# Kernel optimization log

Measured on AMD Instinct MI355X. Metric: run time of the kernel, lower is better.

## Reference

```python
import jax, jax.numpy as jnp
import numpy as np


def setup_inputs() -> dict:
    key = jax.random.key(0)
    ks = jax.random.split(key, 6)
    B, d, S = 256, 512, 196  # batch, hidden dim, spatial locations (14x14)
    return {
        "memory_state": jax.random.normal(ks[0], (B, d), dtype=jnp.float32),
        "ctrl_state": jax.random.normal(ks[1], (B, d), dtype=jnp.float32),
        "kb_proj": jax.random.normal(ks[2], (B, d, S), dtype=jnp.float32),
        "W_concat": jax.random.normal(ks[3], (d, d), dtype=jnp.float32) * (1.0 / np.sqrt(d)),
        "b_concat": jax.random.normal(ks[4], (d,), dtype=jnp.float32) * 0.01,
        "w_attn": jax.random.normal(ks[5], (d,), dtype=jnp.float32) * (1.0 / np.sqrt(d)),
    }


def reference(memory_state, ctrl_state, kb_proj, W_concat, b_concat, w_attn):
    # I_elements: [B, S, d] -- elementwise gating of knowledge base by memory
    I_t = memory_state[:, :, None] * kb_proj           # [B, d, S]
    I_t = jnp.transpose(I_t, (0, 2, 1))                # [B, S, d]
    # concat_layer (torch Linear: x @ W^T + b) + residual with kb_proj
    concat = jnp.einsum('bsd,ed->bse', I_t, W_concat) + b_concat
    concat = concat + jnp.transpose(kb_proj, (0, 2, 1))  # [B, S, d]
    # attention logits: (concat * ctrl) @ w_attn -> [B, S]
    rai = jnp.einsum('bsd,d->bs', concat * ctrl_state[:, None, :], w_attn)
    rvi = jax.nn.softmax(rai, axis=1)                  # [B, S]
    # attention-weighted sum over spatial locations -> [B, d]
    read_vector = jnp.einsum('bs,bds->bd', rvi, kb_proj)
    return read_vector
```

## Files before the change

kernel.cpp:

```cpp
#include <hip/hip_runtime.h>
#include <math.h>

#define B 256
#define D 512
#define S 196
#define NCH 8
#define TC 16
#define NT 13
#define PAD 20

#define BAR() do { asm volatile("s_waitcnt lgkmcnt(0)" ::: "memory"); \
                   __builtin_amdgcn_s_barrier();                      \
                   asm volatile("" ::: "memory"); } while (0)

__global__ __launch_bounds__(256) void k_gemm2(
    const float* __restrict__ ctrl, const float* __restrict__ w_attn,
    const float* __restrict__ W, float* __restrict__ gpart) {
    __shared__ float u_s[64][8];
    const int ce = blockIdx.x >> 6;
    const int dh = (blockIdx.x >> 5) & 1;
    const int b0 = (blockIdx.x & 31) * 8;
    const int t = threadIdx.x;
    const int d = dh * 256 + t;
#pragma unroll
    for (int k = t; k < 512; k += 256) {
        const int j = k & 7, el = k >> 3;
        const int e = ce * 64 + el;
        u_s[el][j] = ctrl[(size_t)(b0 + j) * D + e] * w_attn[e];
    }
    __syncthreads();
    float a[8];
#pragma unroll
    for (int j = 0; j < 8; ++j) a[j] = 0.f;
    for (int e0 = 0; e0 < 64; e0 += 4) {
        float wv[4];
#pragma unroll
        for (int i = 0; i < 4; ++i)
            wv[i] = W[(size_t)(ce * 64 + e0 + i) * D + d];
#pragma unroll
        for (int i = 0; i < 4; ++i) {
            const float4 ua = *(const float4*)&u_s[e0 + i][0];
            const float4 ub = *(const float4*)&u_s[e0 + i][4];
            a[0] += ua.x * wv[i]; a[1] += ua.y * wv[i];
            a[2] += ua.z * wv[i]; a[3] += ua.w * wv[i];
            a[4] += ub.x * wv[i]; a[5] += ub.y * wv[i];
            a[6] += ub.z * wv[i]; a[7] += ub.w * wv[i];
        }
    }
#pragma unroll
    for (int j = 0; j < 8; ++j)
        gpart[((size_t)(b0 + j) * NCH + ce) * D + d] = a[j];
}

__global__ __launch_bounds__(1024, 1) void k_online(
    const float* __restrict__ kb, const float* __restrict__ gpart,
    const float* __restrict__ mem, const float* __restrict__ ctrl,
    const float* __restrict__ w_attn, float* __restrict__ out) {
    __shared__ __align__(16) float tile[2][D][PAD];
    __shared__ __align__(16) float pr[TC][132];
    __shared__ __align__(16) float w_s[TC];
    __shared__ float p_s[D];
    __shared__ float oa[2][D];
    __shared__ float Zs[2];
    const int b = blockIdx.x;
    const int t = threadIdx.x;
    const float* base = kb + (size_t)b * D * S;

    const int ld_d = t >> 2, col_lo = 4 * (t & 3);

    float4 v0 = *(const float4*)(base + (size_t)ld_d * S + col_lo);
    float4 v1 = *(const float4*)(base + (size_t)(ld_d + 256) * S + col_lo);

    if (t < D) {
        float s = 0.f;
#pragma unroll
        for (int ce = 0; ce < NCH; ++ce)
            s += gpart[((size_t)b * NCH + ce) * D + t];
        p_s[t] = mem[(size_t)b * D + t] * s +
                 ctrl[(size_t)b * D + t] * w_attn[t];
    }
    *(float4*)&tile[0][ld_d][col_lo] = v0;
    *(float4*)&tile[0][ld_d + 256][col_lo] = v1;

    float4 rAa = *(const float4*)(base + (size_t)ld_d * S + TC + col_lo);
    float4 rAb = *(const float4*)(base + (size_t)(ld_d + 256) * S + TC + col_lo);
    float4 rBa = *(const float4*)(base + (size_t)ld_d * S + 2 * TC + col_lo);
    float4 rBb = *(const float4*)(base + (size_t)(ld_d + 256) * S + 2 * TC + col_lo);

    BAR();

    const int c2 = t & 7, dg = t >> 3;
    const float pv0 = p_s[dg * 4 + 0], pv1 = p_s[dg * 4 + 1];
    const float pv2 = p_s[dg * 4 + 2], pv3 = p_s[dg * 4 + 3];
    const int dow = t >> 1, sh = t & 1;

    float Zrun = 0.f, oacc = 0.f;

#define BODY(J, CUR, Ra, Rb)                                                  \
    do {                                                                      \
                                    \
        const float2 q0 = *(const float2*)&tile[CUR][dg * 4 + 0][2 * c2];     \
        const float2 q1 = *(const float2*)&tile[CUR][dg * 4 + 1][2 * c2];     \
        const float2 q2 = *(const float2*)&tile[CUR][dg * 4 + 2][2 * c2];     \
        const float2 q3 = *(const float2*)&tile[CUR][dg * 4 + 3][2 * c2];     \
        pr[2 * c2 + 0][dg] =                                                  \
            pv0 * q0.x + pv1 * q1.x + pv2 * q2.x + pv3 * q3.x;                \
        pr[2 * c2 + 1][dg] =                                                  \
            pv0 * q0.y + pv1 * q1.y + pv2 * q2.y + pv3 * q3.y;                \
        BAR();                                                                \
                          \
        if (t < 64) {                                                         \
            const int c = t >> 2, q = t & 3;                                  \
            float s = 0.f;                                                    \
            _Pragma("unroll")                                                 \
            for (int k = 0; k < 8; ++k) {                                     \
                const float4 v = *(const float4*)&pr[c][q * 32 + 4 * k];      \
                s += (v.x + v.y) + (v.z + v.w);                               \
            }                                                                 \
            s += __shfl_xor(s, 1, 64);                                        \
            s += __shfl_xor(s, 2, 64);                                        \
            if (q == 0) w_s[c] = ((J) * TC + c < S) ? __expf(s) : 0.f;        \
        }                                                                     \
        BAR();                                                                \
                          \
        const float4 wA = *(const float4*)&w_s[sh * 8];                       \
        const float4 wB = *(const float4*)&w_s[sh * 8 + 4];                   \
        Zrun += ((wA.x + wA.y) + (wA.z + wA.w)) +                             \
                ((wB.x + wB.y) + (wB.z + wB.w));                              \
        const float4 ta = *(const float4*)&tile[CUR][dow][sh * 8];            \
        const float4 tb = *(const float4*)&tile[CUR][dow][sh * 8 + 4];        \
        oacc += wA.x * ta.x + wA.y * ta.y + wA.z * ta.z + wA.w * ta.w +       \
                wB.x * tb.x + wB.y * tb.y + wB.z * tb.z + wB.w * tb.w;        \
                      \
        if ((J) + 1 < NT) {                                                   \
            *(float4*)&tile[(CUR) ^ 1][ld_d][col_lo] = Ra;                    \
            *(float4*)&tile[(CUR) ^ 1][ld_d + 256][col_lo] = Rb;              \
        }                                                                     \
        if ((J) + 3 < NT) {                                                   \
            const int cq = ((J) + 3) * TC + col_lo;                           \
            if (cq + 3 < S) {                                                 \
                Ra = *(const float4*)(base + (size_t)ld_d * S + cq);          \
                Rb = *(const float4*)(base + (size_t)(ld_d + 256) * S + cq);  \
            } else {                                                          \
                Ra = make_float4(0.f, 0.f, 0.f, 0.f);                         \
                Rb = make_float4(0.f, 0.f, 0.f, 0.f);                         \
            }                                                                 \
        }                                                                     \
        BAR();                                                                \
    } while (0)

    for (int j = 0; j < NT; j += 2) {
        BODY(j, 0, rAa, rAb);
        if (j + 1 < NT) BODY(j + 1, 1, rBa, rBb);
    }
#undef BODY

    oa[sh][dow] = oacc;
    if (t == 0) Zs[0] = Zrun;
    if (t == 1) Zs[1] = Zrun;
    __syncthreads();
    if (t < D)
        out[(size_t)b * D + t] = (oa[0][t] + oa[1][t]) / (Zs[0] + Zs[1]);
}

extern "C" void kernel_launch(void* const* d_in, const int* in_sizes, int n_in,
                              void* d_out, int out_size, void* d_ws, size_t ws_size,
                              hipStream_t stream) {
    const float* mem  = (const float*)d_in[0];
    const float* ctrl = (const float*)d_in[1];
    const float* kb   = (const float*)d_in[2];
    const float* W    = (const float*)d_in[3];
    const float* wat  = (const float*)d_in[5];
    float* out = (float*)d_out;

    float* gpart = (float*)d_ws;

    k_gemm2 <<<512, 256,  0, stream>>>(ctrl, wat, W, gpart);
    k_online<<<B,   1024, 0, stream>>>(kb, gpart, mem, ctrl, wat, out);
}
```

Before: 175.4 us.

## Split spatial axis across two blocks per batch with merge kernel and register-resident tiles

The online-softmax kernel is split so that each batch is handled by two blocks, each covering half of the spatial locations (7 and 6 chunks), and partial outputs and normalizers go to workspace. A new small kernel merges them by summing the partials and dividing. The weighted-sum stage now reads kb values kept in registers instead of the LDS tile, and the LDS tile is single-buffered with padding, so each block needs far less shared memory. The intent is to get more blocks in flight on the GPU, with one extra launch and partial-result traffic as the added cost.

Measured after the change: 228.1 us. 30.0% more time.

```diff
diff --git a/kernel.cpp b/kernel.cpp
--- a/kernel.cpp
+++ b/kernel.cpp
@@ -6,8 +6,8 @@
 #define S 196
 #define NCH 8
 #define TC 16
-#define NT 13
-#define PAD 20
+#define RPAD 17
+#define PPAD 68
 
 #define BAR() do { asm volatile("s_waitcnt lgkmcnt(0)" ::: "memory"); \
                    __builtin_amdgcn_s_barrier();                      \
@@ -52,24 +52,29 @@
         gpart[((size_t)(b0 + j) * NCH + ce) * D + d] = a[j];
 }
 
-__global__ __launch_bounds__(1024, 1) void k_online(
+__global__ __launch_bounds__(1024, 8) void k_half2(
     const float* __restrict__ kb, const float* __restrict__ gpart,
     const float* __restrict__ mem, const float* __restrict__ ctrl,
-    const float* __restrict__ w_attn, float* __restrict__ out) {
-    __shared__ __align__(16) float tile[2][D][PAD];
-    __shared__ __align__(16) float pr[TC][132];
+    const float* __restrict__ w_attn, float* __restrict__ opart,
+    float* __restrict__ zpart) {
+    __shared__ float tile[D][RPAD];
+    __shared__ float pr[TC][PPAD];
+    __shared__ float p_s[D];
     __shared__ __align__(16) float w_s[TC];
-    __shared__ float p_s[D];
-    __shared__ float oa[2][D];
-    __shared__ float Zs[2];
-    const int b = blockIdx.x;
+    const int bid = blockIdx.x;
+    const int b = bid >> 1, h = bid & 1;
+    const int c0 = h ? 112 : 0;
+    const int NTb = h ? 6 : 7;
     const int t = threadIdx.x;
-    const float* base = kb + (size_t)b * D * S;
+    const float* base = kb + (size_t)b * D * S + c0;
 
     const int ld_d = t >> 2, col_lo = 4 * (t & 3);
+    const int col = t & 15, dseg = t >> 4;
 
-    float4 v0 = *(const float4*)(base + (size_t)ld_d * S + col_lo);
-    float4 v1 = *(const float4*)(base + (size_t)(ld_d + 256) * S + col_lo);
+    float4 vA0 = *(const float4*)(base + (size_t)ld_d * S + col_lo);
+    float4 vA1 = *(const float4*)(base + (size_t)(ld_d + 256) * S + col_lo);
+    float4 vB0 = *(const float4*)(base + (size_t)ld_d * S + TC + col_lo);
+    float4 vB1 = *(const float4*)(base + (size_t)(ld_d + 256) * S + TC + col_lo);
 
     if (t < D) {
         float s = 0.f;
@@ -79,88 +84,97 @@
         p_s[t] = mem[(size_t)b * D + t] * s +
                  ctrl[(size_t)b * D + t] * w_attn[t];
     }
-    *(float4*)&tile[0][ld_d][col_lo] = v0;
-    *(float4*)&tile[0][ld_d + 256][col_lo] = v1;
-
-    float4 rAa = *(const float4*)(base + (size_t)ld_d * S + TC + col_lo);
-    float4 rAb = *(const float4*)(base + (size_t)(ld_d + 256) * S + TC + col_lo);
-    float4 rBa = *(const float4*)(base + (size_t)ld_d * S + 2 * TC + col_lo);
-    float4 rBb = *(const float4*)(base + (size_t)(ld_d + 256) * S + 2 * TC + col_lo);
-
+    tile[ld_d][col_lo + 0] = vA0.x; tile[ld_d][col_lo + 1] = vA0.y;
+    tile[ld_d][col_lo + 2] = vA0.z; tile[ld_d][col_lo + 3] = vA0.w;
+    tile[ld_d + 256][col_lo + 0] = vA1.x; tile[ld_d + 256][col_lo + 1] = vA1.y;
+    tile[ld_d + 256][col_lo + 2] = vA1.z; tile[ld_d + 256][col_lo + 3] = vA1.w;
     BAR();
 
-    const int c2 = t & 7, dg = t >> 3;
-    const float pv0 = p_s[dg * 4 + 0], pv1 = p_s[dg * 4 + 1];
-    const float pv2 = p_s[dg * 4 + 2], pv3 = p_s[dg * 4 + 3];
-    const int dow = t >> 1, sh = t & 1;
+    float pv[8];
+#pragma unroll
+    for (int i = 0; i < 8; ++i) pv[i] = p_s[dseg * 8 + i];
 
-    float Zrun = 0.f, oacc = 0.f;
+    float oacc0 = 0.f, oacc1 = 0.f, Zpart = 0.f;
 
-#define BODY(J, CUR, Ra, Rb)                                                  \
-    do {                                                                      \
-                                    \
-        const float2 q0 = *(const float2*)&tile[CUR][dg * 4 + 0][2 * c2];     \
-        const float2 q1 = *(const float2*)&tile[CUR][dg * 4 + 1][2 * c2];     \
-        const float2 q2 = *(const float2*)&tile[CUR][dg * 4 + 2][2 * c2];     \
-        const float2 q3 = *(const float2*)&tile[CUR][dg * 4 + 3][2 * c2];     \
-        pr[2 * c2 + 0][dg] =                                                  \
-            pv0 * q0.x + pv1 * q1.x + pv2 * q2.x + pv3 * q3.x;                \
-        pr[2 * c2 + 1][dg] =                                                  \
-            pv0 * q0.y + pv1 * q1.y + pv2 * q2.y + pv3 * q3.y;                \
-        BAR();                                                                \
-                          \
-        if (t < 64) {                                                         \
-            const int c = t >> 2, q = t & 3;                                  \
-            float s = 0.f;                                                    \
-            _Pragma("unroll")                                                 \
-            for (int k = 0; k < 8; ++k) {                                     \
-                const float4 v = *(const float4*)&pr[c][q * 32 + 4 * k];      \
-                s += (v.x + v.y) + (v.z + v.w);                               \
-            }                                                                 \
-            s += __shfl_xor(s, 1, 64);                                        \
-            s += __shfl_xor(s, 2, 64);                                        \
-            if (q == 0) w_s[c] = ((J) * TC + c < S) ? __expf(s) : 0.f;        \
-        }                                                                     \
-        BAR();                                                                \
-                          \
-        const float4 wA = *(const float4*)&w_s[sh * 8];                       \
-        const float4 wB = *(const float4*)&w_s[sh * 8 + 4];                   \
-        Zrun += ((wA.x + wA.y) + (wA.z + wA.w)) +                             \
-                ((wB.x + wB.y) + (wB.z + wB.w));                              \
-        const float4 ta = *(const float4*)&tile[CUR][dow][sh * 8];            \
-        const float4 tb = *(const float4*)&tile[CUR][dow][sh * 8 + 4];        \
-        oacc += wA.x * ta.x + wA.y * ta.y + wA.z * ta.z + wA.w * ta.w +       \
-                wB.x * tb.x + wB.y * tb.y + wB.z * tb.z + wB.w * tb.w;        \
-                      \
-        if ((J) + 1 < NT) {                                                   \
-            *(float4*)&tile[(CUR) ^ 1][ld_d][col_lo] = Ra;                    \
-            *(float4*)&tile[(CUR) ^ 1][ld_d + 256][col_lo] = Rb;              \
-        }                                                                     \
-        if ((J) + 3 < NT) {                                                   \
-            const int cq = ((J) + 3) * TC + col_lo;                           \
-            if (cq + 3 < S) {                                                 \
-                Ra = *(const float4*)(base + (size_t)ld_d * S + cq);          \
-                Rb = *(const float4*)(base + (size_t)(ld_d + 256) * S + cq);  \
-            } else {                                                          \
-                Ra = make_float4(0.f, 0.f, 0.f, 0.f);                         \
-                Rb = make_float4(0.f, 0.f, 0.f, 0.f);                         \
-            }                                                                 \
-        }                                                                     \
-        BAR();                                                                \
+#define BODY(J, Oa0, Oa1, Pb0, Pb1)                                          \
+    do {                                                                     \
+            \
+        float a = 0.f;                                                       \
+        _Pragma("unroll")                                                    \
+        for (int i = 0; i < 8; ++i) a += pv[i] * tile[dseg * 8 + i][col];    \
+        pr[col][dseg] = a;                                                   \
+        BAR();                                                               \
+          \
+        if (t < 64) {                                                        \
+            const int c = t >> 2, qq = t & 3;                                \
+            const float4 x0 = *(const float4*)&pr[c][qq * 16 + 0];           \
+            const float4 x1 = *(const float4*)&pr[c][qq * 16 + 4];           \
+            const float4 x2 = *(const float4*)&pr[c][qq * 16 + 8];           \
+            const float4 x3 = *(const float4*)&pr[c][qq * 16 + 12];          \
+            float s = ((x0.x + x0.y) + (x0.z + x0.w)) +                      \
+                      ((x1.x + x1.y) + (x1.z + x1.w)) +                      \
+                      ((x2.x + x2.y) + (x2.z + x2.w)) +                      \
+                      ((x3.x + x3.y) + (x3.z + x3.w));                       \
+            s += __shfl_xor(s, 1, 64);                                       \
+            s += __shfl_xor(s, 2, 64);                                       \
+            if (qq == 0)                                                     \
+                w_s[c] = (c0 + (J) * TC + c < S) ? __expf(s) : 0.f;          \
+        }                                                                    \
+        if ((J) + 1 < NTb) {                                                 \
+            tile[ld_d][col_lo + 0] = Pb0.x; tile[ld_d][col_lo + 1] = Pb0.y;  \
+            tile[ld_d][col_lo + 2] = Pb0.z; tile[ld_d][col_lo + 3] = Pb0.w;  \
+            tile[ld_d + 256][col_lo + 0] = Pb1.x;                            \
+            tile[ld_d + 256][col_lo + 1] = Pb1.y;                            \
+            tile[ld_d + 256][col_lo + 2] = Pb1.z;                            \
+            tile[ld_d + 256][col_lo + 3] = Pb1.w;                            \
+        }                                                                    \
+        BAR();                                                               \
+                    \
+        {                                                                    \
+            const float4 w4 = *(const float4*)&w_s[col_lo];                  \
+            Zpart += (w4.x + w4.y) + (w4.z + w4.w);                          \
+            oacc0 += w4.x * Oa0.x + w4.y * Oa0.y +                           \
+                     w4.z * Oa0.z + w4.w * Oa0.w;                            \
+            oacc1 += w4.x * Oa1.x + w4.y * Oa1.y +                           \
+                     w4.z * Oa1.z + w4.w * Oa1.w;                            \
+        }                                                                    \
+            \
+        if ((J) + 2 < NTb) {                                                 \
+            const int cq = ((J) + 2) * TC + col_lo;                          \
+            if (c0 + cq + 3 < S) {                                           \
+                Oa0 = *(const float4*)(base + (size_t)ld_d * S + cq);        \
+                Oa1 = *(const float4*)(base + (size_t)(ld_d + 256) * S + cq);\
+            } else {                                                         \
+                Oa0 = make_float4(0.f, 0.f, 0.f, 0.f);                       \
+                Oa1 = make_float4(0.f, 0.f, 0.f, 0.f);                       \
+            }                                                                \
+        }                                                                    \
     } while (0)
 
-    for (int j = 0; j < NT; j += 2) {
-        BODY(j, 0, rAa, rAb);
-        if (j + 1 < NT) BODY(j + 1, 1, rBa, rBb);
+    for (int j = 0; j < NTb; j += 2) {
+        BODY(j, vA0, vA1, vB0, vB1);
+        if (j + 1 < NTb) BODY(j + 1, vB0, vB1, vA0, vA1);
     }
 #undef BODY
 
-    oa[sh][dow] = oacc;
-    if (t == 0) Zs[0] = Zrun;
-    if (t == 1) Zs[1] = Zrun;
-    __syncthreads();
-    if (t < D)
-        out[(size_t)b * D + t] = (oa[0][t] + oa[1][t]) / (Zs[0] + Zs[1]);
+    oacc0 += __shfl_xor(oacc0, 1, 64); oacc0 += __shfl_xor(oacc0, 2, 64);
+    oacc1 += __shfl_xor(oacc1, 1, 64); oacc1 += __shfl_xor(oacc1, 2, 64);
+    Zpart += __shfl_xor(Zpart, 1, 64); Zpart += __shfl_xor(Zpart, 2, 64);
+    if ((t & 3) == 0) {
+        float* op = opart + ((size_t)h * B + b) * D;
+        op[ld_d]       = oacc0;
+        op[ld_d + 256] = oacc1;
+    }
+    if (t == 0) zpart[h * B + b] = Zpart;
+}
+
+__global__ __launch_bounds__(512) void k_merge(
+    const float* __restrict__ opart, const float* __restrict__ zpart,
+    float* __restrict__ out) {
+    const int b = blockIdx.x, t = threadIdx.x;
+    const float z = zpart[b] + zpart[B + b];
+    out[(size_t)b * D + t] =
+        (opart[(size_t)b * D + t] + opart[((size_t)B + b) * D + t]) / z;
 }
 
 extern "C" void kernel_launch(void* const* d_in, const int* in_sizes, int n_in,
@@ -174,7 +188,10 @@
     float* out = (float*)d_out;
 
     float* gpart = (float*)d_ws;
+    float* opart = gpart + (size_t)B * NCH * D;
+    float* zpart = opart + (size_t)2 * B * D;
 
-    k_gemm2 <<<512, 256,  0, stream>>>(ctrl, wat, W, gpart);
-    k_online<<<B,   1024, 0, stream>>>(kb, gpart, mem, ctrl, wat, out);
+    k_gemm2<<<512,   256,  0, stream>>>(ctrl, wat, W, gpart);
+    k_half2<<<2 * B, 1024, 0, stream>>>(kb, gpart, mem, ctrl, wat, opart, zpart);
+    k_merge<<<B,     512,  0, stream>>>(opart, zpart, out);
 }
```
